# Kernel optimization log

Hardware: AMD Instinct MI355X
Metric: run time of the kernel (lower is better)

The kernel has to match this reference:

```python
import jax, jax.numpy as jnp
from jax import lax
import numpy as np

BOX_SIZE = 64      # box_size
KERNEL = 5         # maxpool kernel (pad=2, stride=1)
THRESH = 0.95
MAX_BOXES = 256    # fixed-shape cap replacing torch nonzero()
NEG = -1e30        # padding value standing in for 'outside the image'


def setup_inputs() -> dict:
    key = jax.random.key(0)
    k1, k2 = jax.random.split(key)
    category_grids = jax.random.uniform(k1, (8, 3, 256, 256), dtype=jnp.float32)
    images = jax.random.normal(k2, (8, 3, 1024, 1024), dtype=jnp.float32)
    return {"category_grids": category_grids, "images": images}


def _maxpool_same(x):
    # nn.MaxPool2d(kernel_size=5, padding=2, stride=1)
    return lax.reduce_window(x, -jnp.inf, lax.max,
                             (1, 1, KERNEL, KERNEL), (1, 1, 1, 1), 'SAME')


def reference(category_grids, images):
    B, C, Hg, Wg = category_grids.shape
    # ---- GridsToBoxes: maxpool-equality peak NMS + threshold ----
    is_peak = (_maxpool_same(category_grids) == category_grids) & (category_grids > THRESH)
    peaks = category_grids * is_peak  # zero everywhere except peaks

    # fixed-shape replacement for nonzero(): per-image top-k over (C*Hg*Wg)
    flat = peaks.reshape(B, -1)
    vals, idx = lax.top_k(flat, MAX_BOXES)          # [B, K]
    valid = vals > 0.0                              # peak values are > THRESH > 0
    rem = idx % (Hg * Wg)
    cy = rem // Wg                                  # [B, K] int32
    cx = rem % Wg

    half = BOX_SIZE // 2
    x1 = cx - half
    y1 = cy - half
    # box_convert cxcywh -> xyxy
    boxes = jnp.stack([x1, y1, cx + half, cy + half], axis=-1).astype(jnp.float32)  # [B,K,4]

    # ---- CenterCrop: roi_pool(images, boxes, output_size=BOX_SIZE) ----
    # torchvision roi_pool: roi_width = x2-x1+1 = BOX_SIZE+1, adaptive max-pooled to BOX_SIZE bins;
    # out-of-image bins give 0. Emulate by padding with NEG and max-gathering fixed bins.
    P = BOX_SIZE + 1
    pad = BOX_SIZE
    padded = jnp.pad(images, ((0, 0), (0, 0), (pad, pad), (pad, pad)),
                     constant_values=NEG)

    def crop_one(img, y, x):  # img: [3, Hp, Wp]
        return lax.dynamic_slice(img, (0, y + pad, x + pad), (img.shape[0], P, P))

    patches = jax.vmap(lambda img, ys, xs:
                       jax.vmap(lambda y, x: crop_one(img, y, x))(ys, xs)
                       )(padded, y1, x1)            # [B, K, 3, P, P]

    # static adaptive-maxpool bin boundaries: bin i covers [floor(i*P/O), ceil((i+1)*P/O))
    O = BOX_SIZE
    i = np.arange(O)
    b0 = np.floor(i * P / O).astype(np.int32)       # bin width is 1 or 2 -> two gathers suffice
    b1 = (np.ceil((i + 1) * P / O) - 1).astype(np.int32)
    rows = jnp.maximum(patches[..., b0, :], patches[..., b1, :])   # pool H: [B,K,3,O,P]
    pooled = jnp.maximum(rows[..., b0], rows[..., b1])             # pool W: [B,K,3,O,O]
    pooled = jnp.where(pooled < NEG * 0.5, 0.0, pooled)            # empty/outside bins -> 0
    pooled = pooled * valid[:, :, None, None, None].astype(pooled.dtype)

    return peaks, boxes, pooled, valid
```

## Files before the change

### kernel.cpp

```cpp
#include <hip/hip_runtime.h>
#include <stdint.h>
#include <math.h>

#define NB 8
#define NC 3
#define HG 256
#define WG 256
#define IMG 1024
#define TOPK 256
#define HALF 32
#define PEAK_THRESH 0.95f
#define NEGV (-1e30f)
#define SELCAP 2048
#define VB_LO 0x3F733334u
#define NBUCK 256
#define BSHIFT 12

#define ROWS_PB 16
#define GRPS (HG / ROWS_PB)
#define PLANES (NB * NC)
#define PK_BLOCKS (PLANES * GRPS)
#define SLOTS 256

typedef float f32x4 __attribute__((ext_vector_type(4)));

#define WS_BCAND_OFF 4096
#define WS_SEL_OFF   (WS_BCAND_OFF + (size_t)PK_BLOCKS * SLOTS * 8)

__global__ void __launch_bounds__(256) peaks_kernel(const float* __restrict__ g,
                                                    float* __restrict__ peaks_out,
                                                    uint32_t* __restrict__ bcnt,
                                                    unsigned long long* __restrict__ bcand) {
    __shared__ float vms[ROWS_PB][WG];
    __shared__ unsigned long long lkeys[SLOTS];
    __shared__ uint32_t lcount;

    int blk   = blockIdx.x;
    int grp   = blk & (GRPS - 1);
    int plane = blk >> 4;
    int c     = plane % NC;
    int y0    = grp * ROWS_PB;
    int x     = threadIdx.x;

    if (x == 0) lcount = 0;

    const float* gc = g + (size_t)plane * (HG * WG);
    float col[ROWS_PB + 4];
#pragma unroll
    for (int d = 0; d < ROWS_PB + 4; ++d) {
        int yy = y0 - 2 + d;
        col[d] = (yy >= 0 && yy < HG) ? gc[yy * WG + x] : -INFINITY;
    }
#pragma unroll
    for (int r = 0; r < ROWS_PB; ++r)
        vms[r][x] = fmaxf(fmaxf(fmaxf(col[r], col[r + 1]), fmaxf(col[r + 2], col[r + 3])),
                          col[r + 4]);
    __syncthreads();

#pragma unroll
    for (int r = 0; r < ROWS_PB; ++r) {
        float v = col[r + 2];
        float h = vms[r][x];
        if (x >= 2)      h = fmaxf(h, vms[r][x - 2]);
        if (x >= 1)      h = fmaxf(h, vms[r][x - 1]);
        if (x <= WG - 2) h = fmaxf(h, vms[r][x + 1]);
        if (x <= WG - 3) h = fmaxf(h, vms[r][x + 2]);
        bool peak = (h == v) && (v > PEAK_THRESH);
        peaks_out[(size_t)plane * (HG * WG) + (y0 + r) * WG + x] = peak ? v : 0.0f;
        if (peak) {
            uint32_t pos = atomicAdd(&lcount, 1u);
            if (pos < SLOTS) {
                int cell = c * (HG * WG) + (y0 + r) * WG + x;
                lkeys[pos] = ((unsigned long long)__float_as_uint(v) << 32) |
                             (uint32_t)(~(uint32_t)cell);
            }
        }
    }
    __syncthreads();
    uint32_t n = min(lcount, (uint32_t)SLOTS);
    if (x == 0) bcnt[blk] = n;
    if ((uint32_t)x < n) bcand[(size_t)blk * SLOTS + x] = lkeys[x];
}

__device__ __forceinline__ void emit_entry(int b, int kk, int idx, int vld,
                                           float* boxes_out, float* valid_out, int4* sel) {
    int rem = idx & 65535;
    int cy = rem >> 8, cx = rem & 255;
    int x1 = cx - HALF, y1 = cy - HALF;
    float4 bo = make_float4((float)x1, (float)y1, (float)(cx + HALF), (float)(cy + HALF));
    *(float4*)(boxes_out + ((size_t)b * TOPK + kk) * 4) = bo;
    valid_out[b * TOPK + kk] = vld ? 1.0f : 0.0f;
    sel[b * TOPK + kk] = make_int4(y1, x1, vld, 0);
}

#define BLKS_PER_IMG (NC * GRPS)

__global__ void __launch_bounds__(1024) topk_kernel(const uint32_t* __restrict__ bcnt,
                                                    const unsigned long long* __restrict__ bcand,
                                                    float* __restrict__ boxes_out,
                                                    float* __restrict__ valid_out,
                                                    int4* __restrict__ sel) {
    __shared__ uint32_t hist[NBUCK];
    __shared__ uint32_t scnts[BLKS_PER_IMG];
    __shared__ unsigned long long skeys[SELCAP];
    __shared__ uint32_t sT, scnt;
    int b = blockIdx.x, t = threadIdx.x;

    if (t < NBUCK) hist[t] = 0;
    if (t < BLKS_PER_IMG) scnts[t] = bcnt[b * BLKS_PER_IMG + t];
    if (t == 0) { sT = 0; scnt = 0; }
    __syncthreads();

    const unsigned long long* cb = bcand + (size_t)b * BLKS_PER_IMG * SLOTS;

    for (int s = t; s < BLKS_PER_IMG * SLOTS; s += 1024) {
        int j = s >> 8, i = s & (SLOTS - 1);
        if ((uint32_t)i < scnts[j]) {
            uint32_t vb = (uint32_t)(cb[(size_t)j * SLOTS + i] >> 32);
            uint32_t bk = (vb - VB_LO) >> BSHIFT;
            if (bk > (NBUCK - 1u)) bk = NBUCK - 1u;
            atomicAdd(&hist[bk], 1u);
        }
    }
    __syncthreads();

    for (int off = 1; off < NBUCK; off <<= 1) {
        uint32_t v = 0;
        if (t < NBUCK) v = hist[t] + ((t + off < NBUCK) ? hist[t + off] : 0u);
        __syncthreads();
        if (t < NBUCK) hist[t] = v;
        __syncthreads();
    }
    if (t < NBUCK) {
        uint32_t st  = hist[t];
        uint32_t stn = (t < NBUCK - 1) ? hist[t + 1] : 0u;
        if (st >= TOPK && stn < TOPK) sT = (uint32_t)t;
    }
    __syncthreads();
    uint32_t T = sT;

    for (int s = t; s < BLKS_PER_IMG * SLOTS; s += 1024) {
        int j = s >> 8, i = s & (SLOTS - 1);
        if ((uint32_t)i < scnts[j]) {
            unsigned long long key = cb[(size_t)j * SLOTS + i];
            uint32_t vb = (uint32_t)(key >> 32);
            uint32_t bk = (vb - VB_LO) >> BSHIFT;
            if (bk > (NBUCK - 1u)) bk = NBUCK - 1u;
            if (bk >= T) {
                uint32_t p = atomicAdd(&scnt, 1u);
                if (p < SELCAP) skeys[p] = key;
            }
        }
    }
    __syncthreads();
    int nsel = (int)min(scnt, (uint32_t)SELCAP);

    if (nsel < TOPK && t < TOPK)
        emit_entry(b, t, t, 0, boxes_out, valid_out, sel);
    __syncthreads();

    for (int p = t; p < nsel; p += 1024) {
        unsigned long long key = skeys[p];
        int rank = 0;
        for (int i = 0; i < nsel; ++i)
            rank += (skeys[i] > key) ? 1 : 0;
        if (rank < TOPK)
            emit_entry(b, rank, (int)(~(uint32_t)key), 1, boxes_out, valid_out, sel);
    }
}

__global__ void __launch_bounds__(256) crop_kernel(const float* __restrict__ images,
                                                   const int4* __restrict__ sel,
                                                   float* __restrict__ pooled) {
    int bid = blockIdx.x;
    int bk  = bid / NC;
    int c   = bid - bk * NC;
    int b   = bk >> 8;
    int4 s = sel[bk];
    int y1 = s.x, x1 = s.y, vld = s.z;

    int t     = threadIdx.x;
    int j0    = (t & 15) * 4;
    int rb    = t >> 4;
    int xa    = x1 & ~3;
    int c0    = x1 & 3;
    const float* img  = images + ((size_t)b * NC + c) * (size_t)(IMG * IMG);
    float*       outc = pooled + (size_t)bid * 4096;

    int yt = y1 + rb * 4;
    float Y[5][8];
    bool fast = (x1 >= 0 && yt >= 0);
    if (fast) {
        const float* p0 = img + (size_t)yt * IMG + (xa + j0);
#pragma unroll
        for (int i = 0; i < 5; ++i) {
            f32x4 lo = *(const f32x4*)(p0 + (size_t)i * IMG);
            f32x4 hi = *(const f32x4*)(p0 + (size_t)i * IMG + 4);
#pragma unroll
            for (int e = 0; e < 4; ++e) { Y[i][e] = lo[e]; Y[i][e + 4] = hi[e]; }
        }
    } else {
#pragma unroll
        for (int i = 0; i < 5; ++i) {
            int yy = yt + i;
            const float* row = img + (size_t)yy * IMG;
            bool yv = (yy >= 0);
#pragma unroll
            for (int k = 0; k < 8; ++k) {
                int xx = xa + j0 + k;
                Y[i][k] = (yv && xx >= 0) ? row[xx] : NEGV;
            }
        }
    }

#pragma unroll
    for (int it = 0; it < 4; ++it) {
        float w[8];
#pragma unroll
        for (int k = 0; k < 8; ++k) w[k] = fmaxf(Y[it][k], Y[it + 1][k]);
        f32x4 o;
#define DO_C0(C0) { _Pragma("unroll") for (int e = 0; e < 4; ++e) o[e] = fmaxf(w[(C0) + e], w[(C0) + e + 1]); }
        switch (c0) {
            case 0: DO_C0(0); break;
            case 1: DO_C0(1); break;
            case 2: DO_C0(2); break;
            default: DO_C0(3); break;
        }
#undef DO_C0
#pragma unroll
        for (int e = 0; e < 4; ++e) {
            float rr = o[e];
            if (!fast) rr = (rr < NEGV * 0.5f) ? 0.0f : rr;
            if (!vld) rr = 0.0f;
            o[e] = rr;
        }
        *(f32x4*)(outc + (rb * 4 + it) * 64 + j0) = o;
    }
}

extern "C" void kernel_launch(void* const* d_in, const int* in_sizes, int n_in,
                              void* d_out, int out_size, void* d_ws, size_t ws_size,
                              hipStream_t stream) {
    const float* grids  = (const float*)d_in[0];
    const float* images = (const float*)d_in[1];

    float* out = (float*)d_out;
    float* peaks_out = out;
    float* boxes_out = out + (size_t)NB * NC * HG * WG;
    float* pooled_out = boxes_out + (size_t)NB * TOPK * 4;
    float* valid_out = pooled_out + (size_t)NB * TOPK * NC * 64 * 64;

    uint32_t* bcnt = (uint32_t*)d_ws;
    unsigned long long* bcand = (unsigned long long*)((char*)d_ws + WS_BCAND_OFF);
    int4* sel = (int4*)((char*)d_ws + WS_SEL_OFF);

    peaks_kernel<<<PK_BLOCKS, 256, 0, stream>>>(grids, peaks_out, bcnt, bcand);

    topk_kernel<<<NB, 1024, 0, stream>>>(bcnt, bcand, boxes_out, valid_out, sel);

    crop_kernel<<<NB * TOPK * NC, 256, 0, stream>>>(images, sel, pooled_out);
}
```

Baseline: 55.93 us.

## Stage crop patch in shared memory and loop channels per block

The crop kernel now loads each 65x68 patch once into LDS with cooperative vectorized loads, instead of having every thread read overlapping 5x8 windows from global memory. One block now handles all three channels of a box in a loop, so there are a third as many blocks. This removes the redundant global reads of overlapping rows but adds LDS traffic and two barriers per channel, and it serializes the channels inside each block, which lowers parallelism.

```diff
diff --git a/kernel.cpp b/kernel.cpp
--- a/kernel.cpp
+++ b/kernel.cpp
@@ -21,6 +21,10 @@
 #define PLANES (NB * NC)
 #define PK_BLOCKS (PLANES * GRPS)
 #define SLOTS 256
+
+#define PROWS 65
+#define PQUADS 17
+#define PSTRIDE 76
 
 typedef float f32x4 __attribute__((ext_vector_type(4)));
 
@@ -172,69 +176,79 @@
 __global__ void __launch_bounds__(256) crop_kernel(const float* __restrict__ images,
                                                    const int4* __restrict__ sel,
                                                    float* __restrict__ pooled) {
-    int bid = blockIdx.x;
-    int bk  = bid / NC;
-    int c   = bid - bk * NC;
-    int b   = bk >> 8;
+    __shared__ float patch[PROWS * PSTRIDE];
+
+    int bk = blockIdx.x;
+    int b  = bk >> 8;
     int4 s = sel[bk];
     int y1 = s.x, x1 = s.y, vld = s.z;
 
-    int t     = threadIdx.x;
-    int j0    = (t & 15) * 4;
-    int rb    = t >> 4;
-    int xa    = x1 & ~3;
-    int c0    = x1 & 3;
-    const float* img  = images + ((size_t)b * NC + c) * (size_t)(IMG * IMG);
-    float*       outc = pooled + (size_t)bid * 4096;
-
-    int yt = y1 + rb * 4;
-    float Y[5][8];
-    bool fast = (x1 >= 0 && yt >= 0);
-    if (fast) {
-        const float* p0 = img + (size_t)yt * IMG + (xa + j0);
+    int t  = threadIdx.x;
+    int j0 = (t & 15) * 4;
+    int rb = t >> 4;
+    int xa = x1 & ~3;
+    int c0 = x1 & 3;
+    bool fast = (x1 >= 0 && y1 >= 0);
+
+    for (int c = 0; c < NC; ++c) {
+        const float* img  = images + ((size_t)b * NC + c) * (size_t)(IMG * IMG);
+        float*       outc = pooled + ((size_t)bk * NC + c) * 4096;
+
+        if (fast) {
+            const float* p0 = img + (size_t)y1 * IMG + xa;
+            for (int i = t; i < PROWS * PQUADS; i += 256) {
+                int row = i / PQUADS, q = i - row * PQUADS;
+                f32x4 v = *(const f32x4*)(p0 + (size_t)row * IMG + q * 4);
+                *(f32x4*)(&patch[row * PSTRIDE + q * 4]) = v;
+            }
+        } else {
+            for (int i = t; i < PROWS * PQUADS; i += 256) {
+                int row = i / PQUADS, q = i - row * PQUADS;
+                int yy = y1 + row;
+                const float* rowp = img + (size_t)yy * IMG;
+                f32x4 v;
+#pragma unroll
+                for (int e = 0; e < 4; ++e) {
+                    int xx = xa + q * 4 + e;
+                    v[e] = (yy >= 0 && xx >= 0) ? rowp[xx] : NEGV;
+                }
+                *(f32x4*)(&patch[row * PSTRIDE + q * 4]) = v;
+            }
+        }
+        __syncthreads();
+
+        float Y[5][8];
 #pragma unroll
         for (int i = 0; i < 5; ++i) {
-            f32x4 lo = *(const f32x4*)(p0 + (size_t)i * IMG);
-            f32x4 hi = *(const f32x4*)(p0 + (size_t)i * IMG + 4);
+            f32x4 lo = *(const f32x4*)(&patch[(rb * 4 + i) * PSTRIDE + j0]);
+            f32x4 hi = *(const f32x4*)(&patch[(rb * 4 + i) * PSTRIDE + j0 + 4]);
 #pragma unroll
             for (int e = 0; e < 4; ++e) { Y[i][e] = lo[e]; Y[i][e + 4] = hi[e]; }
         }
-    } else {
-#pragma unroll
-        for (int i = 0; i < 5; ++i) {
-            int yy = yt + i;
-            const float* row = img + (size_t)yy * IMG;
-            bool yv = (yy >= 0);
-#pragma unroll
-            for (int k = 0; k < 8; ++k) {
-                int xx = xa + j0 + k;
-                Y[i][k] = (yv && xx >= 0) ? row[xx] : NEGV;
-            }
-        }
-    }
-
-#pragma unroll
-    for (int it = 0; it < 4; ++it) {
-        float w[8];
-#pragma unroll
-        for (int k = 0; k < 8; ++k) w[k] = fmaxf(Y[it][k], Y[it + 1][k]);
-        f32x4 o;
+#pragma unroll
+        for (int it = 0; it < 4; ++it) {
+            float w[8];
+#pragma unroll
+            for (int k = 0; k < 8; ++k) w[k] = fmaxf(Y[it][k], Y[it + 1][k]);
+            f32x4 o;
 #define DO_C0(C0) { _Pragma("unroll") for (int e = 0; e < 4; ++e) o[e] = fmaxf(w[(C0) + e], w[(C0) + e + 1]); }
-        switch (c0) {
-            case 0: DO_C0(0); break;
-            case 1: DO_C0(1); break;
-            case 2: DO_C0(2); break;
-            default: DO_C0(3); break;
-        }
+            switch (c0) {
+                case 0: DO_C0(0); break;
+                case 1: DO_C0(1); break;
+                case 2: DO_C0(2); break;
+                default: DO_C0(3); break;
+            }
 #undef DO_C0
 #pragma unroll
-        for (int e = 0; e < 4; ++e) {
-            float rr = o[e];
-            if (!fast) rr = (rr < NEGV * 0.5f) ? 0.0f : rr;
-            if (!vld) rr = 0.0f;
-            o[e] = rr;
-        }
-        *(f32x4*)(outc + (rb * 4 + it) * 64 + j0) = o;
+            for (int e = 0; e < 4; ++e) {
+                float rr = o[e];
+                if (!fast) rr = (rr < NEGV * 0.5f) ? 0.0f : rr;
+                if (!vld) rr = 0.0f;
+                o[e] = rr;
+            }
+            *(f32x4*)(outc + (rb * 4 + it) * 64 + j0) = o;
+        }
+        __syncthreads();
     }
 }
 
@@ -258,5 +272,5 @@
 
     topk_kernel<<<NB, 1024, 0, stream>>>(bcnt, bcand, boxes_out, valid_out, sel);
 
-    crop_kernel<<<NB * TOPK * NC, 256, 0, stream>>>(images, sel, pooled_out);
-}
+    crop_kernel<<<NB * TOPK, 256, 0, stream>>>(images, sel, pooled_out);
+}
```

Result: faster. 54.57 us (-2.4%).
